# Kernel tuning notes

Measured on AMD Instinct MI355X. Metric: run time of the kernel, lower is better.

## Reference

```python
import jax, jax.numpy as jnp
import numpy as np


def setup_inputs() -> dict:
    key = jax.random.key(0)
    k_x, k_g, k_fc, k_pj = jax.random.split(key, 4)
    B, T, C, H, E = 4, 2048, 1024, 2048, 8
    n_layer = 12
    x = jax.random.normal(k_x, (B, T, C), dtype=jnp.float32)
    w_gate = 0.02 * jax.random.normal(k_g, (C, E), dtype=jnp.float32)
    w_fc = 0.02 * jax.random.normal(k_fc, (C, H, E), dtype=jnp.float32)
    w_proj = (0.02 * (2 * n_layer) ** -0.5) * jax.random.normal(k_pj, (H, C, E), dtype=jnp.float32)
    return {"x": x, "w_gate": w_gate, "w_fc": w_fc, "w_proj": w_proj, "top_k": 2}


def reference(x, w_gate, w_fc, w_proj, top_k):
    # x: (B,T,C); w_gate: (C,E); w_fc: (C,H,E); w_proj: (H,C,E)
    E = w_gate.shape[-1]
    gate = jnp.einsum('btc,ce->bte', x, w_gate)                  # gating logits
    top_vals, top_idx = jax.lax.top_k(gate, top_k)               # (B,T,K) — raw logits used as combine weights (as in source)
    # Per-expert combine weight: sum_k top_val_k * onehot(idx_k) — zero for unselected experts.
    # This is mathematically identical to gathering the K expert weight slices per token
    # (the source's gather+einsum) but avoids the (B,T,C,H,K) weight blowup.
    onehot = jax.nn.one_hot(top_idx, E, dtype=x.dtype)           # (B,T,K,E)
    w_e = jnp.einsum('btk,btke->bte', top_vals, onehot)          # (B,T,E)
    h = jax.nn.silu(jnp.einsum('btc,che->bthe', x, w_fc))        # (B,T,H,E)
    o = jnp.einsum('bthe,bte,hce->btc', h, w_e, w_proj)          # weighted expert combine
    return o
```

## Files before the change

### kernel.cpp

```cpp
#include <hip/hip_runtime.h>
#include <hip/hip_bf16.h>


#define NTOK 8192
#define CD   1024
#define HD   2048
#define NE   8
#define NSLOT 16384
#define MT256 10
#define BK   64
#define NT1  (CD / BK)
#define NT2  (HD / BK)
#define PACK_BLOCKS 2048

typedef short  short4_t  __attribute__((ext_vector_type(4)));
typedef short  short8_t  __attribute__((ext_vector_type(8)));
typedef __bf16 bf16x8_t  __attribute__((ext_vector_type(8)));
typedef float  f32x4_t   __attribute__((ext_vector_type(4)));

struct FragArg {
  short8_t v;
  __device__ operator short8_t() const { return v; }
  __device__ operator bf16x8_t() const { return __builtin_bit_cast(bf16x8_t, v); }
};

static __device__ __forceinline__ float b2f(unsigned short u) {
  union { float f; unsigned int i; } w; w.i = ((unsigned int)u) << 16; return w.f;
}
static __device__ __forceinline__ unsigned short f2b(float f) {
  unsigned int u = __float_as_uint(f);
  u += 0x7fffu + ((u >> 16) & 1u);
  return (unsigned short)(u >> 16);
}
static __device__ __forceinline__ void gl2lds16(const void* g, void* l) {
  __builtin_amdgcn_global_load_lds((__attribute__((address_space(1))) void*)g,
                                   (__attribute__((address_space(3))) void*)l,
                                   16, 0, 0);
}

static __device__ __forceinline__ void pack_tile(
    const float* __restrict__ in, unsigned short* __restrict__ out,
    int D0, int D1, int b0, int b1, unsigned short* smem, int t)
{
  int d1i = t & 31, d0q = t >> 5;
  #pragma unroll
  for (int r = 0; r < 4; ++r) {
    int d0i = d0q * 4 + r;
    const float* src = in + ((size_t)(b0 + d0i) * D1 + (b1 + d1i)) * NE;
    float4 v0 = *(const float4*)src;
    float4 v1 = *(const float4*)(src + 4);
    unsigned short* dst0 = &smem[d1i * 40 + d0i];
    dst0[0 * 32 * 40] = f2b(v0.x);
    dst0[1 * 32 * 40] = f2b(v0.y);
    dst0[2 * 32 * 40] = f2b(v0.z);
    dst0[3 * 32 * 40] = f2b(v0.w);
    dst0[4 * 32 * 40] = f2b(v1.x);
    dst0[5 * 32 * 40] = f2b(v1.y);
    dst0[6 * 32 * 40] = f2b(v1.z);
    dst0[7 * 32 * 40] = f2b(v1.w);
  }
  __syncthreads();
  int dchunk = t & 3, d1w = (t >> 2) & 31, ehalf = t >> 7;
  #pragma unroll
  for (int p = 0; p < 4; ++p) {
    int e = ehalf + 2 * p;
    short8_t v = *(const short8_t*)&smem[e * 32 * 40 + d1w * 40 + dchunk * 8];
    *(short8_t*)(out + ((size_t)e * D1 + (b1 + d1w)) * D0 + b0 + dchunk * 8) = v;
  }
}

#define GATE_BLOCKS (NTOK / 4)
__global__ __launch_bounds__(256) void prep_kernel(
    const float* __restrict__ x, const float* __restrict__ wg,
    const float* __restrict__ wfc, const float* __restrict__ wpj,
    unsigned short* __restrict__ xb, unsigned short* __restrict__ wfcp,
    unsigned short* __restrict__ wpjp,
    int* __restrict__ tok_e, float* __restrict__ tok_v,
    int* __restrict__ g_counts)
{
  __shared__ __align__(16) unsigned short lds[NE * 32 * 40];
  __shared__ int hist[NE];
  int t = threadIdx.x;

  if (blockIdx.x < GATE_BLOCKS) {
    if (t < NE) hist[t] = 0;
    __syncthreads();
    int wv = t >> 6, lane = t & 63;
    int tk = blockIdx.x * 4 + wv;
    const float* xr = x + (size_t)tk * CD;
    unsigned short* xbr = xb + (size_t)tk * CD;
    float acc[NE] = {0, 0, 0, 0, 0, 0, 0, 0};
    #pragma unroll
    for (int jj = 0; jj < 4; ++jj) {
      int c0 = (lane + 64 * jj) * 4;
      float4 xv = *(const float4*)(xr + c0);
      short4_t ob;
      ob[0] = (short)f2b(xv.x); ob[1] = (short)f2b(xv.y);
      ob[2] = (short)f2b(xv.z); ob[3] = (short)f2b(xv.w);
      *(short4_t*)(xbr + c0) = ob;
      #pragma unroll
      for (int j = 0; j < 4; ++j) {
        float xf = (j == 0) ? xv.x : (j == 1) ? xv.y : (j == 2) ? xv.z : xv.w;
        const float* wr = wg + (size_t)(c0 + j) * NE;
        float4 w0 = *(const float4*)wr;
        float4 w1 = *(const float4*)(wr + 4);
        acc[0] += xf * w0.x; acc[1] += xf * w0.y;
        acc[2] += xf * w0.z; acc[3] += xf * w0.w;
        acc[4] += xf * w1.x; acc[5] += xf * w1.y;
        acc[6] += xf * w1.z; acc[7] += xf * w1.w;
      }
    }
    #pragma unroll
    for (int off = 32; off >= 1; off >>= 1)
      #pragma unroll
      for (int e = 0; e < NE; ++e) acc[e] += __shfl_down(acc[e], off, 64);
    if (lane == 0) {
      float v1 = -3.0e38f, v2 = -3.0e38f; int i1 = 0, i2 = 1;
      #pragma unroll
      for (int e = 0; e < NE; ++e) {
        float g = acc[e];
        if (g > v1) { v2 = v1; i2 = i1; v1 = g; i1 = e; }
        else if (g > v2) { v2 = g; i2 = e; }
      }
      tok_e[tk * 2] = i1; tok_e[tk * 2 + 1] = i2;
      tok_v[tk * 2] = v1; tok_v[tk * 2 + 1] = v2;
      atomicAdd(&hist[i1], 1); atomicAdd(&hist[i2], 1);
    }
    __syncthreads();
    if (t < NE && hist[t] > 0) atomicAdd(&g_counts[t], hist[t]);
  } else if (blockIdx.x < GATE_BLOCKS + PACK_BLOCKS) {
    int pid = blockIdx.x - GATE_BLOCKS;
    int bx = pid & 63, by = pid >> 6;
    pack_tile(wfc, wfcp, CD, HD, by * 32, bx * 32, lds, t);
  } else {
    int pid = blockIdx.x - GATE_BLOCKS - PACK_BLOCKS;
    int bx = pid & 63, by = pid >> 6;
    pack_tile(wpj, wpjp, HD, CD, bx * 32, by * 32, lds, t);
  }
}

__global__ __launch_bounds__(256) void scatter_kernel(
    const int* __restrict__ tok_e, const float* __restrict__ tok_v,
    const int* __restrict__ g_counts, int* __restrict__ g_cursor,
    int* __restrict__ g_base,
    int* __restrict__ bucket_tok, float* __restrict__ bucket_v,
    int* __restrict__ slot_of)
{
  int gid = blockIdx.x * 256 + threadIdx.x;
  int lane = threadIdx.x & 63;
  int base[NE];
  { int o = 0;
    #pragma unroll
    for (int e = 0; e < NE; ++e) { base[e] = o; o += g_counts[e]; } }
  int e = tok_e[gid];
  unsigned long long lanebit = 1ull << lane;
  int pos = 0;
  #pragma unroll
  for (int ee = 0; ee < NE; ++ee) {
    unsigned long long m = __ballot(e == ee);
    if (e == ee) {
      int leader = __ffsll((long long)m) - 1;
      int cnt = __popcll(m);
      int start = 0;
      if (lane == leader) start = atomicAdd(&g_cursor[ee], cnt);
      start = __shfl(start, leader, 64);
      pos = start + __popcll(m & (lanebit - 1));
    }
  }
  int sl = base[e] + pos;
  bucket_tok[sl] = gid >> 1;
  bucket_v[sl]   = tok_v[gid];
  slot_of[gid]   = sl;
  if (gid < NE) g_base[gid] = base[gid];
}

__global__ __launch_bounds__(512, 2) void gemm1_kernel(
    const unsigned short* __restrict__ xb, const unsigned short* __restrict__ wfcp,
    const int* __restrict__ g_counts, const int* __restrict__ g_base,
    const int* __restrict__ bucket_tok, const float* __restrict__ bucket_v,
    unsigned short* __restrict__ hbuf)
{
  __shared__ __align__(16) unsigned short lsA[2][2][256][32];
  __shared__ __align__(16) unsigned short lsB[2][2][256][32];
  __shared__ int   s_tok[256];
  __shared__ float s_v[256];

  int id = blockIdx.x;
  int e = id & 7;
  int r = id >> 3;
  int nt = r & 7;
  int mt = r >> 3;

  int cnt = g_counts[e];
  int m0 = mt * 256;
  if (m0 >= cnt) return;
  int base = g_base[e];
  int n0 = nt * 256;

  int t = threadIdx.x;
  if (t < 256) {
    int ok = (m0 + t) < cnt;
    s_tok[t] = ok ? bucket_tok[base + m0 + t] : 0;
    s_v[t]   = ok ? bucket_v[base + m0 + t] : 0.0f;
  }
  __syncthreads();

  int lane = t & 63, w = t >> 6;
  int w32 = w * 32;
  int rl0 = w32 + (lane >> 2);
  int rl1 = rl0 + 16;
  int cb  = ((lane & 3) ^ (rl0 & 3)) * 8;
  const unsigned short* aS0 = xb + (size_t)s_tok[rl0] * CD + cb;
  const unsigned short* aS1 = xb + (size_t)s_tok[rl1] * CD + cb;
  const unsigned short* bS0 = wfcp + ((size_t)e * HD + n0 + rl0) * CD + cb;
  const unsigned short* bS1 = wfcp + ((size_t)e * HD + n0 + rl1) * CD + cb;

  #define STG1(tt, kh) do {                                              \
    int _ko = (tt) * BK + (kh) * 32;                                     \
    int _b  = (tt) & 1;                                                  \
    gl2lds16(aS0 + _ko, &lsA[_b][kh][w32][0]);                           \
    gl2lds16(aS1 + _ko, &lsA[_b][kh][w32 + 16][0]);                      \
    gl2lds16(bS0 + _ko, &lsB[_b][kh][w32][0]);                           \
    gl2lds16(bS1 + _ko, &lsB[_b][kh][w32 + 16][0]);                      \
  } while (0)

  int wr = w >> 2, wc = w & 3;
  int ml = lane & 15, kq = lane >> 4;
  int sw8 = (kq ^ (ml & 3)) * 8;

  f32x4_t acc[8][4];
  #pragma unroll
  for (int i = 0; i < 8; ++i)
    #pragma unroll
    for (int j = 0; j < 4; ++j) acc[i][j] = (f32x4_t){0.f, 0.f, 0.f, 0.f};

  STG1(0, 0); STG1(0, 1); STG1(1, 0);
  asm volatile("s_waitcnt vmcnt(8)" ::: "memory");
  __builtin_amdgcn_s_barrier();
  asm volatile("" ::: "memory");

  #pragma unroll 1
  for (int tt = 0; tt < NT1; ++tt) {
    int buf = tt & 1;
    short8_t af[8], bfr[4];
    #pragma unroll
    for (int i = 0; i < 8; ++i)
      af[i]  = *(const short8_t*)&lsA[buf][0][wr * 128 + i * 16 + ml][sw8];
    #pragma unroll
    for (int j = 0; j < 4; ++j)
      bfr[j] = *(const short8_t*)&lsB[buf][0][wc * 64 + j * 16 + ml][sw8];
    if (tt + 1 < NT1) STG1(tt + 1, 1);
    __builtin_amdgcn_s_barrier();
    __builtin_amdgcn_s_setprio(1);
    #pragma unroll
    for (int i = 0; i < 8; ++i)
      #pragma unroll
      for (int j = 0; j < 4; ++j)
        acc[i][j] = __builtin_amdgcn_mfma_f32_16x16x32_bf16(
            FragArg{af[i]}, FragArg{bfr[j]}, acc[i][j], 0, 0, 0);
    __builtin_amdgcn_s_setprio(0);
    if (tt < NT1 - 1) asm volatile("s_waitcnt vmcnt(8)" ::: "memory");
    else              asm volatile("s_waitcnt vmcnt(0)" ::: "memory");
    __builtin_amdgcn_s_barrier();
    asm volatile("" ::: "memory");
    #pragma unroll
    for (int i = 0; i < 8; ++i)
      af[i]  = *(const short8_t*)&lsA[buf][1][wr * 128 + i * 16 + ml][sw8];
    #pragma unroll
    for (int j = 0; j < 4; ++j)
      bfr[j] = *(const short8_t*)&lsB[buf][1][wc * 64 + j * 16 + ml][sw8];
    if (tt + 2 < NT1) STG1(tt + 2, 0);
    __builtin_amdgcn_s_barrier();
    __builtin_amdgcn_s_setprio(1);
    #pragma unroll
    for (int i = 0; i < 8; ++i)
      #pragma unroll
      for (int j = 0; j < 4; ++j)
        acc[i][j] = __builtin_amdgcn_mfma_f32_16x16x32_bf16(
            FragArg{af[i]}, FragArg{bfr[j]}, acc[i][j], 0, 0, 0);
    __builtin_amdgcn_s_setprio(0);
    if (tt + 2 < NT1)      asm volatile("s_waitcnt vmcnt(8)" ::: "memory");
    else if (tt + 1 < NT1) asm volatile("s_waitcnt vmcnt(4)" ::: "memory");
    __builtin_amdgcn_s_barrier();
    asm volatile("" ::: "memory");
  }
  #undef STG1

  #pragma unroll
  for (int i = 0; i < 8; ++i) {
    int rb = wr * 128 + i * 16 + kq * 4;
    #pragma unroll
    for (int r2 = 0; r2 < 4; ++r2) {
      int row = rb + r2;
      if (m0 + row < cnt) {
        float v = s_v[row];
        size_t ro = (size_t)(base + m0 + row) * HD + n0;
        #pragma unroll
        for (int j = 0; j < 4; ++j) {
          float z = acc[i][j][r2];
          float val = v * (z / (1.0f + __expf(-z)));
          hbuf[ro + wc * 64 + j * 16 + ml] = f2b(val);
        }
      }
    }
  }
}

__global__ __launch_bounds__(512, 2) void gemm2_kernel(
    const unsigned short* __restrict__ hbuf, const unsigned short* __restrict__ wpjp,
    const int* __restrict__ g_counts, const int* __restrict__ g_base,
    unsigned short* __restrict__ oslot)
{
  __shared__ __align__(16) unsigned short lsA[2][2][256][32];
  __shared__ __align__(16) unsigned short lsB[2][2][256][32];

  int id = blockIdx.x;
  int e = id & 7;
  int r = id >> 3;
  int nt = r & 3;
  int mt = r >> 2;

  int cnt = g_counts[e];
  int m0 = mt * 256;
  if (m0 >= cnt) return;
  int base = g_base[e];
  int n0 = nt * 256;

  int t = threadIdx.x;
  int lane = t & 63, w = t >> 6;
  int w32 = w * 32;
  int rl0 = w32 + (lane >> 2);
  int rl1 = rl0 + 16;
  int cb  = ((lane & 3) ^ (rl0 & 3)) * 8;
  const unsigned short* aS0 = hbuf + ((size_t)(base + m0 + rl0)) * HD + cb;
  const unsigned short* aS1 = hbuf + ((size_t)(base + m0 + rl1)) * HD + cb;
  const unsigned short* bS0 = wpjp + ((size_t)e * CD + n0 + rl0) * HD + cb;
  const unsigned short* bS1 = wpjp + ((size_t)e * CD + n0 + rl1) * HD + cb;

  #define STG2(tt, kh) do {                                              \
    int _ko = (tt) * BK + (kh) * 32;                                     \
    int _b  = (tt) & 1;                                                  \
    gl2lds16(aS0 + _ko, &lsA[_b][kh][w32][0]);                           \
    gl2lds16(aS1 + _ko, &lsA[_b][kh][w32 + 16][0]);                      \
    gl2lds16(bS0 + _ko, &lsB[_b][kh][w32][0]);                           \
    gl2lds16(bS1 + _ko, &lsB[_b][kh][w32 + 16][0]);                      \
  } while (0)

  int wr = w >> 2, wc = w & 3;
  int ml = lane & 15, kq = lane >> 4;
  int sw8 = (kq ^ (ml & 3)) * 8;

  f32x4_t acc[8][4];
  #pragma unroll
  for (int i = 0; i < 8; ++i)
    #pragma unroll
    for (int j = 0; j < 4; ++j) acc[i][j] = (f32x4_t){0.f, 0.f, 0.f, 0.f};

  asm volatile("s_waitcnt vmcnt(0)" ::: "memory");
  STG2(0, 0); STG2(0, 1); STG2(1, 0);
  asm volatile("s_waitcnt vmcnt(8)" ::: "memory");
  __builtin_amdgcn_s_barrier();
  asm volatile("" ::: "memory");

  #pragma unroll 1
  for (int tt = 0; tt < NT2; ++tt) {
    int buf = tt & 1;
    short8_t af[8], bfr[4];
    #pragma unroll
    for (int i = 0; i < 8; ++i)
      af[i]  = *(const short8_t*)&lsA[buf][0][wr * 128 + i * 16 + ml][sw8];
    #pragma unroll
    for (int j = 0; j < 4; ++j)
      bfr[j] = *(const short8_t*)&lsB[buf][0][wc * 64 + j * 16 + ml][sw8];
    if (tt + 1 < NT2) STG2(tt + 1, 1);
    __builtin_amdgcn_s_barrier();
    __builtin_amdgcn_s_setprio(1);
    #pragma unroll
    for (int i = 0; i < 8; ++i)
      #pragma unroll
      for (int j = 0; j < 4; ++j)
        acc[i][j] = __builtin_amdgcn_mfma_f32_16x16x32_bf16(
            FragArg{af[i]}, FragArg{bfr[j]}, acc[i][j], 0, 0, 0);
    __builtin_amdgcn_s_setprio(0);
    if (tt < NT2 - 1) asm volatile("s_waitcnt vmcnt(8)" ::: "memory");
    else              asm volatile("s_waitcnt vmcnt(0)" ::: "memory");
    __builtin_amdgcn_s_barrier();
    asm volatile("" ::: "memory");
    #pragma unroll
    for (int i = 0; i < 8; ++i)
      af[i]  = *(const short8_t*)&lsA[buf][1][wr * 128 + i * 16 + ml][sw8];
    #pragma unroll
    for (int j = 0; j < 4; ++j)
      bfr[j] = *(const short8_t*)&lsB[buf][1][wc * 64 + j * 16 + ml][sw8];
    if (tt + 2 < NT2) STG2(tt + 2, 0);
    __builtin_amdgcn_s_barrier();
    __builtin_amdgcn_s_setprio(1);
    #pragma unroll
    for (int i = 0; i < 8; ++i)
      #pragma unroll
      for (int j = 0; j < 4; ++j)
        acc[i][j] = __builtin_amdgcn_mfma_f32_16x16x32_bf16(
            FragArg{af[i]}, FragArg{bfr[j]}, acc[i][j], 0, 0, 0);
    __builtin_amdgcn_s_setprio(0);
    if (tt + 2 < NT2)      asm volatile("s_waitcnt vmcnt(8)" ::: "memory");
    else if (tt + 1 < NT2) asm volatile("s_waitcnt vmcnt(4)" ::: "memory");
    __builtin_amdgcn_s_barrier();
    asm volatile("" ::: "memory");
  }
  #undef STG2

  #pragma unroll
  for (int i = 0; i < 8; ++i) {
    int rb = wr * 128 + i * 16 + kq * 4;
    #pragma unroll
    for (int r2 = 0; r2 < 4; ++r2) {
      int row = rb + r2;
      if (m0 + row < cnt) {
        size_t ro = (size_t)(base + m0 + row) * CD + n0;
        #pragma unroll
        for (int j = 0; j < 4; ++j)
          oslot[ro + wc * 64 + j * 16 + ml] = f2b(acc[i][j][r2]);
      }
    }
  }
}

__global__ __launch_bounds__(256) void combine_kernel(
    const unsigned short* __restrict__ oslot, const int* __restrict__ slot_of,
    float* __restrict__ out)
{
  int gid = blockIdx.x * 256 + threadIdx.x;
  int tk = gid >> 7;
  int ch = (gid & 127) * 8;
  int s0 = slot_of[tk * 2], s1 = slot_of[tk * 2 + 1];
  short8_t a = *(const short8_t*)(oslot + (size_t)s0 * CD + ch);
  short8_t b = *(const short8_t*)(oslot + (size_t)s1 * CD + ch);
  float* op = out + (size_t)tk * CD + ch;
  float4 o0, o1;
  o0.x = b2f((unsigned short)a[0]) + b2f((unsigned short)b[0]);
  o0.y = b2f((unsigned short)a[1]) + b2f((unsigned short)b[1]);
  o0.z = b2f((unsigned short)a[2]) + b2f((unsigned short)b[2]);
  o0.w = b2f((unsigned short)a[3]) + b2f((unsigned short)b[3]);
  o1.x = b2f((unsigned short)a[4]) + b2f((unsigned short)b[4]);
  o1.y = b2f((unsigned short)a[5]) + b2f((unsigned short)b[5]);
  o1.z = b2f((unsigned short)a[6]) + b2f((unsigned short)b[6]);
  o1.w = b2f((unsigned short)a[7]) + b2f((unsigned short)b[7]);
  *(float4*)op = o0;
  *(float4*)(op + 4) = o1;
}

extern "C" void kernel_launch(void* const* d_in, const int* in_sizes, int n_in,
                              void* d_out, int out_size, void* d_ws, size_t ws_size,
                              hipStream_t stream)
{
  const float* x   = (const float*)d_in[0];
  const float* wg  = (const float*)d_in[1];
  const float* wfc = (const float*)d_in[2];
  const float* wpj = (const float*)d_in[3];
  float* out = (float*)d_out;

  char* w = (char*)d_ws;
  unsigned short* wfcp  = (unsigned short*)w; w += (size_t)NE * HD * CD * 2;
  unsigned short* wpjp  = (unsigned short*)w; w += (size_t)NE * CD * HD * 2;
  unsigned short* xb    = (unsigned short*)w; w += (size_t)NTOK * CD * 2;
  unsigned short* hbuf  = (unsigned short*)w; w += (size_t)NSLOT * HD * 2;
  unsigned short* oslot = (unsigned short*)w; w += (size_t)NSLOT * CD * 2;
  int*   tok_e      = (int*)w;   w += NSLOT * 4;
  float* tok_v      = (float*)w; w += NSLOT * 4;
  int*   slot_of    = (int*)w;   w += NSLOT * 4;
  int*   bucket_tok = (int*)w;   w += NSLOT * 4;
  float* bucket_v   = (float*)w; w += NSLOT * 4;
  int*   g_counts   = (int*)w;   w += NE * 4;
  int*   g_cursor   = (int*)w;   w += NE * 4;
  int*   g_base     = (int*)w;   w += 256;

  hipMemsetAsync(g_counts, 0, 2 * NE * sizeof(int), stream);
  prep_kernel<<<GATE_BLOCKS + 2 * PACK_BLOCKS, 256, 0, stream>>>(
      x, wg, wfc, wpj, xb, wfcp, wpjp, tok_e, tok_v, g_counts);
  scatter_kernel<<<NSLOT / 256, 256, 0, stream>>>(
      tok_e, tok_v, g_counts, g_cursor, g_base, bucket_tok, bucket_v, slot_of);
  gemm1_kernel<<<(HD / 256) * MT256 * NE, 512, 0, stream>>>(
      xb, wfcp, g_counts, g_base, bucket_tok, bucket_v, hbuf);
  gemm2_kernel<<<(CD / 256) * MT256 * NE, 512, 0, stream>>>(
      hbuf, wpjp, g_counts, g_base, oslot);
  combine_kernel<<<(NTOK * CD / 8) / 256, 256, 0, stream>>>(oslot, slot_of, out);
}
```

Baseline: 493.9 us.

## Restructure GEMM main loop into finer-grained interleaved load/MFMA stages

Reworks the software pipeline in both expert GEMM kernels. Global-to-LDS stages for the A and B tiles are issued separately, and each K-half of MFMA work is split into two 4x4 sub-blocks with a stage issued between them. Staging now prefetches one tile ahead with full double-buffering rather than a half-tile-ahead scheme, and there are fewer barriers per iteration. The aim is to hide memory latency better, cut barrier stalls and lower fragment register pressure, at the risk of a shorter prefetch distance and more exposed LDS reads.

```diff
diff --git a/kernel.cpp b/kernel.cpp
--- a/kernel.cpp
+++ b/kernel.cpp
@@ -215,13 +215,15 @@
   const unsigned short* bS0 = wfcp + ((size_t)e * HD + n0 + rl0) * CD + cb;
   const unsigned short* bS1 = wfcp + ((size_t)e * HD + n0 + rl1) * CD + cb;
 
-  #define STG1(tt, kh) do {                                              \
+  #define STGA1(tt, kh) do {                                             \
     int _ko = (tt) * BK + (kh) * 32;                                     \
-    int _b  = (tt) & 1;                                                  \
-    gl2lds16(aS0 + _ko, &lsA[_b][kh][w32][0]);                           \
-    gl2lds16(aS1 + _ko, &lsA[_b][kh][w32 + 16][0]);                      \
-    gl2lds16(bS0 + _ko, &lsB[_b][kh][w32][0]);                           \
-    gl2lds16(bS1 + _ko, &lsB[_b][kh][w32 + 16][0]);                      \
+    gl2lds16(aS0 + _ko, &lsA[(tt) & 1][kh][w32][0]);                     \
+    gl2lds16(aS1 + _ko, &lsA[(tt) & 1][kh][w32 + 16][0]);                \
+  } while (0)
+  #define STGB1(tt, kh) do {                                             \
+    int _ko = (tt) * BK + (kh) * 32;                                     \
+    gl2lds16(bS0 + _ko, &lsB[(tt) & 1][kh][w32][0]);                     \
+    gl2lds16(bS1 + _ko, &lsB[(tt) & 1][kh][w32 + 16][0]);                \
   } while (0)
 
   int wr = w >> 2, wc = w & 3;
@@ -234,57 +236,76 @@
     #pragma unroll
     for (int j = 0; j < 4; ++j) acc[i][j] = (f32x4_t){0.f, 0.f, 0.f, 0.f};
 
-  STG1(0, 0); STG1(0, 1); STG1(1, 0);
-  asm volatile("s_waitcnt vmcnt(8)" ::: "memory");
-  __builtin_amdgcn_s_barrier();
-  asm volatile("" ::: "memory");
+  STGA1(0, 0); STGB1(0, 0); STGA1(0, 1); STGB1(0, 1);
 
   #pragma unroll 1
   for (int tt = 0; tt < NT1; ++tt) {
     int buf = tt & 1;
-    short8_t af[8], bfr[4];
-    #pragma unroll
-    for (int i = 0; i < 8; ++i)
+    short8_t af[4], bfr[4];
+    asm volatile("s_waitcnt vmcnt(4)" ::: "memory");
+    __builtin_amdgcn_s_barrier();
+    asm volatile("" ::: "memory");
+    #pragma unroll
+    for (int i = 0; i < 4; ++i)
       af[i]  = *(const short8_t*)&lsA[buf][0][wr * 128 + i * 16 + ml][sw8];
     #pragma unroll
     for (int j = 0; j < 4; ++j)
       bfr[j] = *(const short8_t*)&lsB[buf][0][wc * 64 + j * 16 + ml][sw8];
-    if (tt + 1 < NT1) STG1(tt + 1, 1);
-    __builtin_amdgcn_s_barrier();
-    __builtin_amdgcn_s_setprio(1);
-    #pragma unroll
-    for (int i = 0; i < 8; ++i)
+    if (tt + 1 < NT1) STGA1(tt + 1, 0);
+    __builtin_amdgcn_s_setprio(1);
+    #pragma unroll
+    for (int i = 0; i < 4; ++i)
       #pragma unroll
       for (int j = 0; j < 4; ++j)
         acc[i][j] = __builtin_amdgcn_mfma_f32_16x16x32_bf16(
             FragArg{af[i]}, FragArg{bfr[j]}, acc[i][j], 0, 0, 0);
     __builtin_amdgcn_s_setprio(0);
-    if (tt < NT1 - 1) asm volatile("s_waitcnt vmcnt(8)" ::: "memory");
+    #pragma unroll
+    for (int i = 0; i < 4; ++i)
+      af[i]  = *(const short8_t*)&lsA[buf][0][wr * 128 + 64 + i * 16 + ml][sw8];
+    if (tt + 1 < NT1) STGB1(tt + 1, 0);
+    __builtin_amdgcn_s_setprio(1);
+    #pragma unroll
+    for (int i = 0; i < 4; ++i)
+      #pragma unroll
+      for (int j = 0; j < 4; ++j)
+        acc[4 + i][j] = __builtin_amdgcn_mfma_f32_16x16x32_bf16(
+            FragArg{af[i]}, FragArg{bfr[j]}, acc[4 + i][j], 0, 0, 0);
+    __builtin_amdgcn_s_setprio(0);
+    if (tt + 1 < NT1) asm volatile("s_waitcnt vmcnt(4)" ::: "memory");
     else              asm volatile("s_waitcnt vmcnt(0)" ::: "memory");
     __builtin_amdgcn_s_barrier();
     asm volatile("" ::: "memory");
     #pragma unroll
-    for (int i = 0; i < 8; ++i)
+    for (int i = 0; i < 4; ++i)
       af[i]  = *(const short8_t*)&lsA[buf][1][wr * 128 + i * 16 + ml][sw8];
     #pragma unroll
     for (int j = 0; j < 4; ++j)
       bfr[j] = *(const short8_t*)&lsB[buf][1][wc * 64 + j * 16 + ml][sw8];
-    if (tt + 2 < NT1) STG1(tt + 2, 0);
-    __builtin_amdgcn_s_barrier();
-    __builtin_amdgcn_s_setprio(1);
-    #pragma unroll
-    for (int i = 0; i < 8; ++i)
+    if (tt + 1 < NT1) STGA1(tt + 1, 1);
+    __builtin_amdgcn_s_setprio(1);
+    #pragma unroll
+    for (int i = 0; i < 4; ++i)
       #pragma unroll
       for (int j = 0; j < 4; ++j)
         acc[i][j] = __builtin_amdgcn_mfma_f32_16x16x32_bf16(
             FragArg{af[i]}, FragArg{bfr[j]}, acc[i][j], 0, 0, 0);
     __builtin_amdgcn_s_setprio(0);
-    if (tt + 2 < NT1)      asm volatile("s_waitcnt vmcnt(8)" ::: "memory");
-    else if (tt + 1 < NT1) asm volatile("s_waitcnt vmcnt(4)" ::: "memory");
-    __builtin_amdgcn_s_barrier();
-    asm volatile("" ::: "memory");
-  }
-  #undef STG1
+    #pragma unroll
+    for (int i = 0; i < 4; ++i)
+      af[i]  = *(const short8_t*)&lsA[buf][1][wr * 128 + 64 + i * 16 + ml][sw8];
+    if (tt + 1 < NT1) STGB1(tt + 1, 1);
+    __builtin_amdgcn_s_setprio(1);
+    #pragma unroll
+    for (int i = 0; i < 4; ++i)
+      #pragma unroll
+      for (int j = 0; j < 4; ++j)
+        acc[4 + i][j] = __builtin_amdgcn_mfma_f32_16x16x32_bf16(
+            FragArg{af[i]}, FragArg{bfr[j]}, acc[4 + i][j], 0, 0, 0);
+    __builtin_amdgcn_s_setprio(0);
+  }
+  #undef STGA1
+  #undef STGB1
 
   #pragma unroll
   for (int i = 0; i < 8; ++i) {
@@ -337,13 +358,15 @@
   const unsigned short* bS0 = wpjp + ((size_t)e * CD + n0 + rl0) * HD + cb;
   const unsigned short* bS1 = wpjp + ((size_t)e * CD + n0 + rl1) * HD + cb;
 
-  #define STG2(tt, kh) do {                                              \
+  #define STGA2(tt, kh) do {                                             \
     int _ko = (tt) * BK + (kh) * 32;                                     \
-    int _b  = (tt) & 1;                                                  \
-    gl2lds16(aS0 + _ko, &lsA[_b][kh][w32][0]);                           \
-    gl2lds16(aS1 + _ko, &lsA[_b][kh][w32 + 16][0]);                      \
-    gl2lds16(bS0 + _ko, &lsB[_b][kh][w32][0]);                           \
-    gl2lds16(bS1 + _ko, &lsB[_b][kh][w32 + 16][0]);                      \
+    gl2lds16(aS0 + _ko, &lsA[(tt) & 1][kh][w32][0]);                     \
+    gl2lds16(aS1 + _ko, &lsA[(tt) & 1][kh][w32 + 16][0]);                \
+  } while (0)
+  #define STGB2(tt, kh) do {                                             \
+    int _ko = (tt) * BK + (kh) * 32;                                     \
+    gl2lds16(bS0 + _ko, &lsB[(tt) & 1][kh][w32][0]);                     \
+    gl2lds16(bS1 + _ko, &lsB[(tt) & 1][kh][w32 + 16][0]);                \
   } while (0)
 
   int wr = w >> 2, wc = w & 3;
@@ -357,57 +380,76 @@
     for (int j = 0; j < 4; ++j) acc[i][j] = (f32x4_t){0.f, 0.f, 0.f, 0.f};
 
   asm volatile("s_waitcnt vmcnt(0)" ::: "memory");
-  STG2(0, 0); STG2(0, 1); STG2(1, 0);
-  asm volatile("s_waitcnt vmcnt(8)" ::: "memory");
-  __builtin_amdgcn_s_barrier();
-  asm volatile("" ::: "memory");
+  STGA2(0, 0); STGB2(0, 0); STGA2(0, 1); STGB2(0, 1);
 
   #pragma unroll 1
   for (int tt = 0; tt < NT2; ++tt) {
     int buf = tt & 1;
-    short8_t af[8], bfr[4];
-    #pragma unroll
-    for (int i = 0; i < 8; ++i)
+    short8_t af[4], bfr[4];
+    asm volatile("s_waitcnt vmcnt(4)" ::: "memory");
+    __builtin_amdgcn_s_barrier();
+    asm volatile("" ::: "memory");
+    #pragma unroll
+    for (int i = 0; i < 4; ++i)
       af[i]  = *(const short8_t*)&lsA[buf][0][wr * 128 + i * 16 + ml][sw8];
     #pragma unroll
     for (int j = 0; j < 4; ++j)
       bfr[j] = *(const short8_t*)&lsB[buf][0][wc * 64 + j * 16 + ml][sw8];
-    if (tt + 1 < NT2) STG2(tt + 1, 1);
-    __builtin_amdgcn_s_barrier();
-    __builtin_amdgcn_s_setprio(1);
-    #pragma unroll
-    for (int i = 0; i < 8; ++i)
+    if (tt + 1 < NT2) STGA2(tt + 1, 0);
+    __builtin_amdgcn_s_setprio(1);
+    #pragma unroll
+    for (int i = 0; i < 4; ++i)
       #pragma unroll
       for (int j = 0; j < 4; ++j)
         acc[i][j] = __builtin_amdgcn_mfma_f32_16x16x32_bf16(
             FragArg{af[i]}, FragArg{bfr[j]}, acc[i][j], 0, 0, 0);
     __builtin_amdgcn_s_setprio(0);
-    if (tt < NT2 - 1) asm volatile("s_waitcnt vmcnt(8)" ::: "memory");
+    #pragma unroll
+    for (int i = 0; i < 4; ++i)
+      af[i]  = *(const short8_t*)&lsA[buf][0][wr * 128 + 64 + i * 16 + ml][sw8];
+    if (tt + 1 < NT2) STGB2(tt + 1, 0);
+    __builtin_amdgcn_s_setprio(1);
+    #pragma unroll
+    for (int i = 0; i < 4; ++i)
+      #pragma unroll
+      for (int j = 0; j < 4; ++j)
+        acc[4 + i][j] = __builtin_amdgcn_mfma_f32_16x16x32_bf16(
+            FragArg{af[i]}, FragArg{bfr[j]}, acc[4 + i][j], 0, 0, 0);
+    __builtin_amdgcn_s_setprio(0);
+    if (tt + 1 < NT2) asm volatile("s_waitcnt vmcnt(4)" ::: "memory");
     else              asm volatile("s_waitcnt vmcnt(0)" ::: "memory");
     __builtin_amdgcn_s_barrier();
     asm volatile("" ::: "memory");
     #pragma unroll
-    for (int i = 0; i < 8; ++i)
+    for (int i = 0; i < 4; ++i)
       af[i]  = *(const short8_t*)&lsA[buf][1][wr * 128 + i * 16 + ml][sw8];
     #pragma unroll
     for (int j = 0; j < 4; ++j)
       bfr[j] = *(const short8_t*)&lsB[buf][1][wc * 64 + j * 16 + ml][sw8];
-    if (tt + 2 < NT2) STG2(tt + 2, 0);
-    __builtin_amdgcn_s_barrier();
-    __builtin_amdgcn_s_setprio(1);
-    #pragma unroll
-    for (int i = 0; i < 8; ++i)
+    if (tt + 1 < NT2) STGA2(tt + 1, 1);
+    __builtin_amdgcn_s_setprio(1);
+    #pragma unroll
+    for (int i = 0; i < 4; ++i)
       #pragma unroll
       for (int j = 0; j < 4; ++j)
         acc[i][j] = __builtin_amdgcn_mfma_f32_16x16x32_bf16(
             FragArg{af[i]}, FragArg{bfr[j]}, acc[i][j], 0, 0, 0);
     __builtin_amdgcn_s_setprio(0);
-    if (tt + 2 < NT2)      asm volatile("s_waitcnt vmcnt(8)" ::: "memory");
-    else if (tt + 1 < NT2) asm volatile("s_waitcnt vmcnt(4)" ::: "memory");
-    __builtin_amdgcn_s_barrier();
-    asm volatile("" ::: "memory");
-  }
-  #undef STG2
+    #pragma unroll
+    for (int i = 0; i < 4; ++i)
+      af[i]  = *(const short8_t*)&lsA[buf][1][wr * 128 + 64 + i * 16 + ml][sw8];
+    if (tt + 1 < NT2) STGB2(tt + 1, 1);
+    __builtin_amdgcn_s_setprio(1);
+    #pragma unroll
+    for (int i = 0; i < 4; ++i)
+      #pragma unroll
+      for (int j = 0; j < 4; ++j)
+        acc[4 + i][j] = __builtin_amdgcn_mfma_f32_16x16x32_bf16(
+            FragArg{af[i]}, FragArg{bfr[j]}, acc[4 + i][j], 0, 0, 0);
+    __builtin_amdgcn_s_setprio(0);
+  }
+  #undef STGA2
+  #undef STGB2
 
   #pragma unroll
   for (int i = 0; i < 8; ++i) {
```

Measured after the change: 468.2 us. -5.2%, faster.
